# Performance work log

Hardware: AMD Instinct MI355X
Metric: run time of the kernel (lower is better)

The kernel has to match this reference:

```python
import jax, jax.numpy as jnp
import numpy as np

EPS = 1e-6


def _greedy_kcenter_select(cosine, k):
    """Greedy diversity selection (k-center) exactly matching SLAMFormer.Pruner.

    cosine: [L, L] distance matrix (1 - cosine similarity).
    k: static Python int, number of tokens to keep.
    Returns sorted int32 indices of shape [k].
    """
    # torch.topk(cosine, 2, dim=0, largest=False).values[1]: second-smallest per column.
    two_smallest = -jax.lax.top_k(-cosine.T, 2)[0]  # [L, 2], ascending per column
    initial_scores = two_smallest[:, 1]              # [L]
    first = jnp.argmax(initial_scores)
    scores0 = cosine[first].at[first].set(-jnp.inf)  # running min-distance to selected set

    def step(scores, _):
        idx = jnp.argmax(scores)
        scores = jnp.minimum(scores, cosine[idx]).at[idx].set(-jnp.inf)
        return scores, idx

    _, rest = jax.lax.scan(step, scores0, None, length=k - 1)
    sel = jnp.concatenate([first[None], rest])
    return jnp.sort(sel)


def setup_inputs() -> dict:
    key = jax.random.key(0)
    L, C = 4096, 1024  # patch tokens per frame x decoder dim (dinov2-large decoder)
    x = jax.random.normal(key, (L, C), dtype=jnp.float32)
    return {
        "visual_feature_vectors": x,
        "image_feature_length": L,
        "threshold_terms": 1024,  # round(0.25 * L), DivPrune default ratio
    }


def reference(visual_feature_vectors, image_feature_length, threshold_terms):
    x = visual_feature_vectors
    # pairwise_cosine_similarity with clamp_min(1e-6) on the row norms
    norm = jnp.maximum(jnp.linalg.norm(x, axis=1, keepdims=True), EPS)
    xn = x / norm
    cosine = 1.0 - xn @ xn.T  # [L, L] distance matrix
    k = max(1, min(int(threshold_terms), int(image_feature_length)))
    sel = _greedy_kcenter_select(cosine, k)
    return sel, cosine
```

## Files before the change

### kernel.cpp

```cpp
#include <hip/hip_runtime.h>
#include <math.h>

__global__ void rownorm_kernel(const float* __restrict__ x,
                               float* __restrict__ rnorm, int C) {
    int row = blockIdx.x;
    const float4* xr = (const float4*)(x + (size_t)row * C);
    int n4 = C >> 2;
    float s = 0.f;
    for (int c = threadIdx.x; c < n4; c += blockDim.x) {
        float4 v = xr[c];
        s += v.x * v.x + v.y * v.y + v.z * v.z + v.w * v.w;
    }
    for (int off = 32; off > 0; off >>= 1) s += __shfl_down(s, off, 64);
    __shared__ float red[4];
    int lane = threadIdx.x & 63, wid = threadIdx.x >> 6;
    if (lane == 0) red[wid] = s;
    __syncthreads();
    if (threadIdx.x == 0) {
        float t = red[0] + red[1] + red[2] + red[3];
        float n = fmaxf(sqrtf(t), 1e-6f);
        rnorm[row] = 1.0f / n;
    }
}

#define BM 128
#define BN 128
#define BK 32

__global__ __launch_bounds__(256) void cosine_gemm(
        const float* __restrict__ x, const float* __restrict__ rnorm,
        float* __restrict__ cosine, int L, int C) {
    __shared__ float As[BK][BM + 4];
    __shared__ float Bs[BK][BN + 4];
    const int tid = threadIdx.x;
    const int i0 = blockIdx.y * BM;
    const int j0 = blockIdx.x * BN;
    const int tr = (tid >> 4) << 3;
    const int tc = (tid & 15) << 3;
    const int lr = tid >> 3;
    const int lc = (tid & 7) << 2;
    float acc[8][8] = {};

    for (int k0 = 0; k0 < C; k0 += BK) {
#pragma unroll
        for (int q = 0; q < 4; ++q) {
            int r = lr + q * 32;
            float ra = rnorm[i0 + r];
            float4 va = *(const float4*)(x + (size_t)(i0 + r) * C + k0 + lc);
            As[lc + 0][r] = va.x * ra;
            As[lc + 1][r] = va.y * ra;
            As[lc + 2][r] = va.z * ra;
            As[lc + 3][r] = va.w * ra;
            float rb = rnorm[j0 + r];
            float4 vb = *(const float4*)(x + (size_t)(j0 + r) * C + k0 + lc);
            Bs[lc + 0][r] = vb.x * rb;
            Bs[lc + 1][r] = vb.y * rb;
            Bs[lc + 2][r] = vb.z * rb;
            Bs[lc + 3][r] = vb.w * rb;
        }
        __syncthreads();
#pragma unroll
        for (int kk = 0; kk < BK; ++kk) {
            float a[8], b[8];
#pragma unroll
            for (int m = 0; m < 8; ++m) a[m] = As[kk][tr + m];
#pragma unroll
            for (int n = 0; n < 8; ++n) b[n] = Bs[kk][tc + n];
#pragma unroll
            for (int m = 0; m < 8; ++m)
#pragma unroll
                for (int n = 0; n < 8; ++n)
                    acc[m][n] = fmaf(a[m], b[n], acc[m][n]);
        }
        __syncthreads();
    }
#pragma unroll
    for (int m = 0; m < 8; ++m) {
        float* crow = cosine + (size_t)(i0 + tr + m) * L + j0 + tc;
        float4 o0 = {1.f - acc[m][0], 1.f - acc[m][1], 1.f - acc[m][2], 1.f - acc[m][3]};
        float4 o1 = {1.f - acc[m][4], 1.f - acc[m][5], 1.f - acc[m][6], 1.f - acc[m][7]};
        ((float4*)crow)[0] = o0;
        ((float4*)crow)[1] = o1;
    }
}

__global__ void twosmallest_kernel(const float* __restrict__ cosine,
                                   float* __restrict__ min2, int L) {
    int row = blockIdx.x;
    const float4* r4 = (const float4*)(cosine + (size_t)row * L);
    float4 v0 = r4[threadIdx.x];
    float4 v1 = r4[threadIdx.x + 256];
    float4 v2 = r4[threadIdx.x + 512];
    float4 v3 = r4[threadIdx.x + 768];

#define PAIR_INIT(M1, M2, V)                                   \
    float M1 = fminf(V.x, V.y), M2 = fmaxf(V.x, V.y);          \
    { float _n1 = fminf(M1, V.z); M2 = fminf(M2, fmaxf(M1, V.z)); M1 = _n1; \
      _n1 = fminf(M1, V.w); M2 = fminf(M2, fmaxf(M1, V.w)); M1 = _n1; }
    PAIR_INIT(a1, a2, v0)
    PAIR_INIT(b1, b2, v1)
    PAIR_INIT(c1, c2, v2)
    PAIR_INIT(d1, d2, v3)
#undef PAIR_INIT
    float m1 = fminf(a1, b1), m2 = fminf(fmaxf(a1, b1), fminf(a2, b2));
    float n1 = fminf(c1, d1), n2 = fminf(fmaxf(c1, d1), fminf(c2, d2));
    float t1 = fminf(m1, n1), t2 = fminf(fmaxf(m1, n1), fminf(m2, n2));
    float m1r = t1, m2r = t2;

    for (int off = 32; off > 0; off >>= 1) {
        float om1 = __shfl_down(m1r, off, 64);
        float om2 = __shfl_down(m2r, off, 64);
        float nm1 = fminf(m1r, om1);
        float nm2 = fminf(fmaxf(m1r, om1), fminf(m2r, om2));
        m1r = nm1; m2r = nm2;
    }
    __shared__ float s1[4], s2[4];
    int lane = threadIdx.x & 63, wid = threadIdx.x >> 6;
    if (lane == 0) { s1[wid] = m1r; s2[wid] = m2r; }
    __syncthreads();
    if (threadIdx.x == 0) {
        float x1 = s1[0], x2 = s2[0];
        for (int w = 1; w < 4; ++w) {
            float y1 = s1[w], y2 = s2[w];
            float z2 = fminf(fmaxf(x1, y1), fminf(x2, y2));
            x1 = fminf(x1, y1);
            x2 = z2;
        }
        min2[row] = x2;
    }
}

#define FOR16(X) X(0) X(1) X(2) X(3) X(4) X(5) X(6) X(7) \
                 X(8) X(9) X(10) X(11) X(12) X(13) X(14) X(15)

#define ARGMAX16(BV, BJ)                                                      \
  do {                                                                        \
    float _t0,_t1,_t2,_t3,_t4,_t5,_t6,_t7;                                    \
    int _u0,_u1,_u2,_u3,_u4,_u5,_u6,_u7;                                      \
    bool _g;                                                                  \
    _g = sc1  > sc0;  _t0 = _g ? sc1  : sc0;  _u0 = _g ? base+1  : base+0;    \
    _g = sc3  > sc2;  _t1 = _g ? sc3  : sc2;  _u1 = _g ? base+3  : base+2;    \
    _g = sc5  > sc4;  _t2 = _g ? sc5  : sc4;  _u2 = _g ? base+5  : base+4;    \
    _g = sc7  > sc6;  _t3 = _g ? sc7  : sc6;  _u3 = _g ? base+7  : base+6;    \
    _g = sc9  > sc8;  _t4 = _g ? sc9  : sc8;  _u4 = _g ? base+9  : base+8;    \
    _g = sc11 > sc10; _t5 = _g ? sc11 : sc10; _u5 = _g ? base+11 : base+10;   \
    _g = sc13 > sc12; _t6 = _g ? sc13 : sc12; _u6 = _g ? base+13 : base+12;   \
    _g = sc15 > sc14; _t7 = _g ? sc15 : sc14; _u7 = _g ? base+15 : base+14;   \
    _g = _t1 > _t0; _t0 = _g ? _t1 : _t0; _u0 = _g ? _u1 : _u0;               \
    _g = _t3 > _t2; _t2 = _g ? _t3 : _t2; _u2 = _g ? _u3 : _u2;               \
    _g = _t5 > _t4; _t4 = _g ? _t5 : _t4; _u4 = _g ? _u5 : _u4;               \
    _g = _t7 > _t6; _t6 = _g ? _t7 : _t6; _u6 = _g ? _u7 : _u6;               \
    _g = _t2 > _t0; _t0 = _g ? _t2 : _t0; _u0 = _g ? _u2 : _u0;               \
    _g = _t6 > _t4; _t4 = _g ? _t6 : _t4; _u4 = _g ? _u6 : _u4;               \
    _g = _t4 > _t0; BV = _g ? _t4 : _t0; BJ = _g ? _u4 : _u0;                 \
  } while (0)

#define DPP_FMAX(V, CTRL)                                                     \
  do {                                                                        \
    int _b = __builtin_amdgcn_update_dpp(                                     \
        __float_as_int(V), __float_as_int(V), (CTRL), 0xf, 0xf, false);       \
    (V) = fmaxf((V), __int_as_float(_b));                                     \
  } while (0)

static __device__ __forceinline__ void wave_argmax(float bv, int bj,
                                                   float& wv, int& wj) {
    float v = bv;
    DPP_FMAX(v, 0x111);
    DPP_FMAX(v, 0x112);
    DPP_FMAX(v, 0x114);
    DPP_FMAX(v, 0x118);
    DPP_FMAX(v, 0x142);
    DPP_FMAX(v, 0x143);
    float wmax = __int_as_float(
        __builtin_amdgcn_readlane(__float_as_int(v), 63));
    unsigned long long m = __ballot(bv == wmax);
    int lowlane = __ffsll((unsigned long long)m) - 1;
    wj = __builtin_amdgcn_readlane(bj, lowlane);
    wv = wmax;
}

__global__ __launch_bounds__(256) void greedy_kernel(
        const float* __restrict__ cosine, const float* __restrict__ min2,
        float* __restrict__ sel_out, int L, int k) {
    const int tid = threadIdx.x;
    const int lane = tid & 63, wid = tid >> 6;
    __shared__ __align__(16) float sv[2][4];
    __shared__ __align__(16) int si[2][4];
    __shared__ int wsum[4];
    const int base = tid << 4;

#define DECL_SC(i) float sc##i;
    FOR16(DECL_SC)

    float bv; int bj;

    {
        const float4* m4 = (const float4*)min2 + (tid << 2);
        float4 q0 = m4[0], q1 = m4[1], q2 = m4[2], q3 = m4[3];
        sc0 = q0.x;  sc1 = q0.y;  sc2 = q0.z;  sc3 = q0.w;
        sc4 = q1.x;  sc5 = q1.y;  sc6 = q1.z;  sc7 = q1.w;
        sc8 = q2.x;  sc9 = q2.y;  sc10 = q2.z; sc11 = q2.w;
        sc12 = q3.x; sc13 = q3.y; sc14 = q3.z; sc15 = q3.w;
    }
    ARGMAX16(bv, bj);
    {
        float wv; int wj;
        wave_argmax(bv, bj, wv, wj);
        if (lane == 0) { sv[0][wid] = wv; si[0][wid] = wj; }
    }
    __syncthreads();
    int first;
    {
        float4 cv4 = *(const float4*)&sv[0][0];
        int4 ci4 = *(const int4*)&si[0][0];
        float wv = cv4.x; int wi = ci4.x;
        if (cv4.y > wv || (cv4.y == wv && ci4.y < wi)) { wv = cv4.y; wi = ci4.y; }
        if (cv4.z > wv || (cv4.z == wv && ci4.z < wi)) { wv = cv4.z; wi = ci4.z; }
        if (cv4.w > wv || (cv4.w == wv && ci4.w < wi)) { wv = cv4.w; wi = ci4.w; }
        first = wi;
    }
    {
        const float4* rp = (const float4*)(cosine + (size_t)first * L) + (tid << 2);
        float4 q0 = rp[0], q1 = rp[1], q2 = rp[2], q3 = rp[3];
        int sl = ((first >> 4) == tid) ? (first & 15) : -1;
        sc0  = (sl == 0)  ? -INFINITY : q0.x;
        sc1  = (sl == 1)  ? -INFINITY : q0.y;
        sc2  = (sl == 2)  ? -INFINITY : q0.z;
        sc3  = (sl == 3)  ? -INFINITY : q0.w;
        sc4  = (sl == 4)  ? -INFINITY : q1.x;
        sc5  = (sl == 5)  ? -INFINITY : q1.y;
        sc6  = (sl == 6)  ? -INFINITY : q1.z;
        sc7  = (sl == 7)  ? -INFINITY : q1.w;
        sc8  = (sl == 8)  ? -INFINITY : q2.x;
        sc9  = (sl == 9)  ? -INFINITY : q2.y;
        sc10 = (sl == 10) ? -INFINITY : q2.z;
        sc11 = (sl == 11) ? -INFINITY : q2.w;
        sc12 = (sl == 12) ? -INFINITY : q3.x;
        sc13 = (sl == 13) ? -INFINITY : q3.y;
        sc14 = (sl == 14) ? -INFINITY : q3.z;
        sc15 = (sl == 15) ? -INFINITY : q3.w;
    }
    ARGMAX16(bv, bj);

    float pf = 0.f, dummy = 0.f;
    int p = 1;
    for (int it = 0; it < k - 1; ++it) {
        float wv; int wj;
        wave_argmax(bv, bj, wv, wj);
        dummy += pf;
        if (lane == 0) { sv[p][wid] = wv; si[p][wid] = wj; }
        __syncthreads();
        float4 cv4 = *(const float4*)&sv[p][0];
        int4 ci4 = *(const int4*)&si[p][0];
        p ^= 1;
        float cwv = cv4.x; int wi = ci4.x; int wsl = 0;
        if (cv4.y > cwv || (cv4.y == cwv && ci4.y < wi)) { cwv = cv4.y; wi = ci4.y; wsl = 1; }
        if (cv4.z > cwv || (cv4.z == cwv && ci4.z < wi)) { cwv = cv4.z; wi = ci4.z; wsl = 2; }
        if (cv4.w > cwv || (cv4.w == cwv && ci4.w < wi)) { cwv = cv4.w; wi = ci4.w; wsl = 3; }
        const float4* rp = (const float4*)(cosine + (size_t)wi * L) + (tid << 2);
        float4 q0 = rp[0], q1 = rp[1], q2 = rp[2], q3 = rp[3];
        {
            float e0 = (wsl == 0) ? -INFINITY : cv4.x;
            float e1 = (wsl == 1) ? -INFINITY : cv4.y;
            float e2 = (wsl == 2) ? -INFINITY : cv4.z;
            float e3 = (wsl == 3) ? -INFINITY : cv4.w;
            float rv = e0; int ri = ci4.x;
            if (e1 > rv) { rv = e1; ri = ci4.y; }
            if (e2 > rv) { rv = e2; ri = ci4.z; }
            if (e3 > rv) { rv = e3; ri = ci4.w; }
            pf = *(cosine + (size_t)ri * L + (tid << 4));
        }
        int sl = ((wi >> 4) == tid) ? (wi & 15) : -1;
        sc0  = (sl == 0)  ? -INFINITY : fminf(sc0, q0.x);
        sc1  = (sl == 1)  ? -INFINITY : fminf(sc1, q0.y);
        sc2  = (sl == 2)  ? -INFINITY : fminf(sc2, q0.z);
        sc3  = (sl == 3)  ? -INFINITY : fminf(sc3, q0.w);
        sc4  = (sl == 4)  ? -INFINITY : fminf(sc4, q1.x);
        sc5  = (sl == 5)  ? -INFINITY : fminf(sc5, q1.y);
        sc6  = (sl == 6)  ? -INFINITY : fminf(sc6, q1.z);
        sc7  = (sl == 7)  ? -INFINITY : fminf(sc7, q1.w);
        sc8  = (sl == 8)  ? -INFINITY : fminf(sc8, q2.x);
        sc9  = (sl == 9)  ? -INFINITY : fminf(sc9, q2.y);
        sc10 = (sl == 10) ? -INFINITY : fminf(sc10, q2.z);
        sc11 = (sl == 11) ? -INFINITY : fminf(sc11, q2.w);
        sc12 = (sl == 12) ? -INFINITY : fminf(sc12, q3.x);
        sc13 = (sl == 13) ? -INFINITY : fminf(sc13, q3.y);
        sc14 = (sl == 14) ? -INFINITY : fminf(sc14, q3.z);
        sc15 = (sl == 15) ? -INFINITY : fminf(sc15, q3.w);
        ARGMAX16(bv, bj);
    }
    asm volatile("" :: "v"(dummy), "v"(pf));

    unsigned flags = 0; int cnt = 0;
#define FLAGBIT(i) if (sc##i == -INFINITY) { flags |= (1u << i); ++cnt; }
    FOR16(FLAGBIT)
    int incl = cnt;
#pragma unroll
    for (int off = 1; off < 64; off <<= 1) {
        int n = __shfl_up(incl, off, 64);
        if (lane >= off) incl += n;
    }
    if (lane == 63) wsum[wid] = incl;
    __syncthreads();
    int off0 = 0;
#pragma unroll
    for (int w = 0; w < 4; ++w)
        if (w < wid) off0 += wsum[w];
    int pos = off0 + incl - cnt;
#pragma unroll
    for (int j = 0; j < 16; ++j)
        if ((flags >> j) & 1) sel_out[pos++] = (float)(base + j);
}

extern "C" void kernel_launch(void* const* d_in, const int* in_sizes, int n_in,
                              void* d_out, int out_size, void* d_ws, size_t ws_size,
                              hipStream_t stream) {
    const float* x = (const float*)d_in[0];

    long long L = (long long)floor(sqrt((double)out_size));
    while (L * L > (long long)out_size) --L;
    while ((L + 1) * (L + 1) <= (long long)out_size) ++L;
    long long k = (long long)out_size - L * L;
    long long C = (long long)in_sizes[0] / L;

    float* sel = (float*)d_out;
    float* cosine = (float*)d_out + k;
    float* rnorm = (float*)d_ws;
    float* min2 = rnorm + L;

    rownorm_kernel<<<(int)L, 256, 0, stream>>>(x, rnorm, (int)C);
    dim3 g2((int)(L / BN), (int)(L / BM));
    cosine_gemm<<<g2, 256, 0, stream>>>(x, rnorm, cosine, (int)L, (int)C);
    twosmallest_kernel<<<(int)L, 256, 0, stream>>>(cosine, min2, (int)L);
    greedy_kernel<<<1, 256, 0, stream>>>(cosine, min2, sel, (int)L, (int)k);
}
```

Baseline: 1.270 ms.

## Exploit cosine symmetry in GEMM and prefetch two candidate rows in greedy loop

The cosine GEMM now computes only upper-triangular tiles and writes each tile's transpose to the mirrored position, which roughly halves the FLOPs. The transposed stores are strided, one row per n, so write coalescing is worse. The greedy selection loop now issues volatile prefetch loads for the runner-up and third-best wave candidates' rows, replacing the single dummy-accumulated prefetch, to warm the cache for the next iteration. It also drops the index tie-break in the cross-wave argmax comparisons, which could change which index is selected when values are exactly equal.

```diff
diff --git a/kernel.cpp b/kernel.cpp
--- a/kernel.cpp
+++ b/kernel.cpp
@@ -30,6 +30,7 @@
 __global__ __launch_bounds__(256) void cosine_gemm(
         const float* __restrict__ x, const float* __restrict__ rnorm,
         float* __restrict__ cosine, int L, int C) {
+    if (blockIdx.x < blockIdx.y) return;
     __shared__ float As[BK][BM + 4];
     __shared__ float Bs[BK][BN + 4];
     const int tid = threadIdx.x;
@@ -82,6 +83,16 @@
         ((float4*)crow)[0] = o0;
         ((float4*)crow)[1] = o1;
     }
+    if (i0 != j0) {
+#pragma unroll
+        for (int n = 0; n < 8; ++n) {
+            float* trow = cosine + (size_t)(j0 + tc + n) * L + i0 + tr;
+            float4 t0 = {1.f - acc[0][n], 1.f - acc[1][n], 1.f - acc[2][n], 1.f - acc[3][n]};
+            float4 t1 = {1.f - acc[4][n], 1.f - acc[5][n], 1.f - acc[6][n], 1.f - acc[7][n]};
+            ((float4*)trow)[0] = t0;
+            ((float4*)trow)[1] = t1;
+        }
+    }
 }
 
 __global__ void twosmallest_kernel(const float* __restrict__ cosine,
@@ -104,8 +115,7 @@
 #undef PAIR_INIT
     float m1 = fminf(a1, b1), m2 = fminf(fmaxf(a1, b1), fminf(a2, b2));
     float n1 = fminf(c1, d1), n2 = fminf(fmaxf(c1, d1), fminf(c2, d2));
-    float t1 = fminf(m1, n1), t2 = fminf(fmaxf(m1, n1), fminf(m2, n2));
-    float m1r = t1, m2r = t2;
+    float m1r = fminf(m1, n1), m2r = fminf(fmaxf(m1, n1), fminf(m2, n2));
 
     for (int off = 32; off > 0; off >>= 1) {
         float om1 = __shfl_down(m1r, off, 64);
@@ -214,9 +224,9 @@
         float4 cv4 = *(const float4*)&sv[0][0];
         int4 ci4 = *(const int4*)&si[0][0];
         float wv = cv4.x; int wi = ci4.x;
-        if (cv4.y > wv || (cv4.y == wv && ci4.y < wi)) { wv = cv4.y; wi = ci4.y; }
-        if (cv4.z > wv || (cv4.z == wv && ci4.z < wi)) { wv = cv4.z; wi = ci4.z; }
-        if (cv4.w > wv || (cv4.w == wv && ci4.w < wi)) { wv = cv4.w; wi = ci4.w; }
+        if (cv4.y > wv) { wv = cv4.y; wi = ci4.y; }
+        if (cv4.z > wv) { wv = cv4.z; wi = ci4.z; }
+        if (cv4.w > wv) { wv = cv4.w; wi = ci4.w; }
         first = wi;
     }
     {
@@ -242,21 +252,19 @@
     }
     ARGMAX16(bv, bj);
 
-    float pf = 0.f, dummy = 0.f;
     int p = 1;
     for (int it = 0; it < k - 1; ++it) {
         float wv; int wj;
         wave_argmax(bv, bj, wv, wj);
-        dummy += pf;
         if (lane == 0) { sv[p][wid] = wv; si[p][wid] = wj; }
         __syncthreads();
         float4 cv4 = *(const float4*)&sv[p][0];
         int4 ci4 = *(const int4*)&si[p][0];
         p ^= 1;
         float cwv = cv4.x; int wi = ci4.x; int wsl = 0;
-        if (cv4.y > cwv || (cv4.y == cwv && ci4.y < wi)) { cwv = cv4.y; wi = ci4.y; wsl = 1; }
-        if (cv4.z > cwv || (cv4.z == cwv && ci4.z < wi)) { cwv = cv4.z; wi = ci4.z; wsl = 2; }
-        if (cv4.w > cwv || (cv4.w == cwv && ci4.w < wi)) { cwv = cv4.w; wi = ci4.w; wsl = 3; }
+        if (cv4.y > cwv) { cwv = cv4.y; wi = ci4.y; wsl = 1; }
+        if (cv4.z > cwv) { cwv = cv4.z; wi = ci4.z; wsl = 2; }
+        if (cv4.w > cwv) { cwv = cv4.w; wi = ci4.w; wsl = 3; }
         const float4* rp = (const float4*)(cosine + (size_t)wi * L) + (tid << 2);
         float4 q0 = rp[0], q1 = rp[1], q2 = rp[2], q3 = rp[3];
         {
@@ -264,11 +272,22 @@
             float e1 = (wsl == 1) ? -INFINITY : cv4.y;
             float e2 = (wsl == 2) ? -INFINITY : cv4.z;
             float e3 = (wsl == 3) ? -INFINITY : cv4.w;
-            float rv = e0; int ri = ci4.x;
-            if (e1 > rv) { rv = e1; ri = ci4.y; }
-            if (e2 > rv) { rv = e2; ri = ci4.z; }
-            if (e3 > rv) { rv = e3; ri = ci4.w; }
-            pf = *(cosine + (size_t)ri * L + (tid << 4));
+            float rv = e0; int ri = ci4.x; int rsl = 0;
+            if (e1 > rv) { rv = e1; ri = ci4.y; rsl = 1; }
+            if (e2 > rv) { rv = e2; ri = ci4.z; rsl = 2; }
+            if (e3 > rv) { rv = e3; ri = ci4.w; rsl = 3; }
+            float f0 = (rsl == 0) ? -INFINITY : e0;
+            float f1 = (rsl == 1) ? -INFINITY : e1;
+            float f2 = (rsl == 2) ? -INFINITY : e2;
+            float f3 = (rsl == 3) ? -INFINITY : e3;
+            float rv2 = f0; int ri2 = ci4.x;
+            if (f1 > rv2) { rv2 = f1; ri2 = ci4.y; }
+            if (f2 > rv2) { rv2 = f2; ri2 = ci4.z; }
+            if (f3 > rv2) { rv2 = f3; ri2 = ci4.w; }
+            volatile const float* pp1 = cosine + (size_t)ri * L + (tid << 4);
+            volatile const float* pp2 = cosine + (size_t)ri2 * L + (tid << 4);
+            (void)*pp1;
+            (void)*pp2;
         }
         int sl = ((wi >> 4) == tid) ? (wi & 15) : -1;
         sc0  = (sl == 0)  ? -INFINITY : fminf(sc0, q0.x);
@@ -289,7 +308,6 @@
         sc15 = (sl == 15) ? -INFINITY : fminf(sc15, q3.w);
         ARGMAX16(bv, bj);
     }
-    asm volatile("" :: "v"(dummy), "v"(pf));
 
     unsigned flags = 0; int cnt = 0;
 #define FLAGBIT(i) if (sc##i == -INFINITY) { flags |= (1u << i); ++cnt; }
```

New measurement: 1.718 ms. 1.35x slower.
